# Performance work log

Measured on AMD Instinct MI355X. Metric: run time of the kernel, lower is better.

The kernel has to match this reference:

```python
import jax, jax.numpy as jnp
import numpy as np

R = 5            # num_relations
NEG_SLOPE = 0.2
N1 = 30000       # layer0 target count
N2 = 15000       # layer1 target count


def brgcn_conv(x_src, x_tgt, edge_index, edge_type, Wj, Wi, att_j, att_i,
               Wq, Wk, Wv, sw, sb, Wrel, heads, outc):
    """One BRGCNConv layer: per-relation GAT edge softmax + bilevel relation attention."""
    N = x_tgt.shape[0]
    hc = heads * outc
    hj = (x_src @ Wj).reshape(-1, heads, outc)   # [Ns,H,C]
    hi = (x_tgt @ Wi).reshape(-1, heads, outc)   # [N,H,C]
    src, tgt = edge_index[0], edge_index[1]
    xj = hj[src]                                  # [E,H,C]
    xi = hi[tgt]                                  # [E,H,C]
    # relation-specific attention logits per edge
    aj = jnp.sum(att_j[edge_type] * xj, axis=-1)  # [E,H]
    ai = jnp.sum(att_i[edge_type] * xi, axis=-1)  # [E,H]
    alpha = jax.nn.leaky_relu(aj + ai, NEG_SLOPE)
    # edge softmax grouped by (target node, relation) == per-relation propagate
    seg = tgt * R + edge_type                     # [E]
    nseg = N * R
    amax = jax.ops.segment_max(alpha, seg, num_segments=nseg)
    amax = jnp.where(jnp.isfinite(amax), amax, 0.0)
    ex = jnp.exp(alpha - amax[seg])
    den = jax.ops.segment_sum(ex, seg, num_segments=nseg)
    w = ex / jnp.maximum(den[seg], 1e-16)         # [E,H]
    msg = (w[:, :, None] * xj).reshape(-1, hc)    # [E,H*C]
    z = jax.ops.segment_sum(msg, seg, num_segments=nseg)
    z = z.reshape(N, R, hc).transpose(1, 0, 2)    # [R,N,H*C]; zero rows where no edges
    # per-relation Q/K/V
    q = jnp.einsum('rnd,rde->rne', z, Wq).reshape(R, N, heads, outc)
    k = jnp.einsum('rnd,rde->rne', z, Wk).reshape(R, N, heads, outc)
    v = jnp.einsum('rnd,rde->rne', z, Wv).reshape(R, N, heads, outc)
    # bilevel relation attention: psi[r,s,n,h] = <q_r, k_s>
    psi = jnp.einsum('rnhc,snhc->rsnh', q, k)
    mask = (psi == 0) & (jnp.sum(psi, axis=1, keepdims=True) != 0)
    prob = jax.nn.softmax(jnp.where(mask, -jnp.inf, psi), axis=1)
    delta = jnp.einsum('rsnh,snhc->rnhc', prob, v).reshape(R, N, hc)
    out = jnp.einsum('rnd,r->nd', delta, Wrel[:, 0])
    # single node type -> node_self[0] applied to every target node
    return out + x_tgt @ sw + sb


def setup_inputs() -> dict:
    key = jax.random.key(0)
    ks = jax.random.split(key, 32)
    H0, C0, H1, C1 = 4, 64, 1, 40
    IN, HC0 = 128, H0 * C0
    NG, N0 = 200000, 100000
    E0, E1 = 300000, 150000
    f = lambda k, s: jax.random.normal(k, s, dtype=jnp.float32) * 0.05
    return dict(
        n_id=jax.random.randint(ks[1], (N0,), 0, NG),
        local_node_idx=jax.random.randint(ks[2], (NG,), 0, NG),
        node_type=jnp.zeros((NG,), dtype=jnp.int32),
        edge_index0=jax.random.randint(ks[3], (2, E0), 0, N1),
        edge_type0=jax.random.randint(ks[4], (E0,), 0, R),
        edge_index1=jax.random.randint(ks[5], (2, E1), 0, N2),
        edge_type1=jax.random.randint(ks[6], (E1,), 0, R),
        emb=f(ks[0], (NG, IN)),
        Wj0=f(ks[7], (IN, HC0)), Wi0=f(ks[8], (IN, HC0)),
        att_j0=f(ks[9], (R, H0, C0)), att_i0=f(ks[10], (R, H0, C0)),
        Wq0=f(ks[11], (R, HC0, HC0)), Wk0=f(ks[12], (R, HC0, HC0)), Wv0=f(ks[13], (R, HC0, HC0)),
        sw0=f(ks[14], (IN, HC0)), sb0=f(ks[15], (HC0,)), Wrel0=f(ks[16], (R, 1)),
        Wj1=f(ks[17], (HC0, C1)), Wi1=f(ks[18], (HC0, C1)),
        att_j1=f(ks[19], (R, H1, C1)), att_i1=f(ks[20], (R, H1, C1)),
        Wq1=f(ks[21], (R, C1, C1)), Wk1=f(ks[22], (R, C1, C1)), Wv1=f(ks[23], (R, C1, C1)),
        sw1=f(ks[24], (HC0, C1)), sb1=f(ks[25], (C1,)), Wrel1=f(ks[26], (R, 1)),
    )


def reference(n_id, local_node_idx, node_type, edge_index0, edge_type0,
              edge_index1, edge_type1, emb,
              Wj0, Wi0, att_j0, att_i0, Wq0, Wk0, Wv0, sw0, sb0, Wrel0,
              Wj1, Wi1, att_j1, att_i1, Wq1, Wk1, Wv1, sw1, sb1, Wrel1):
    # group_input: single node type, all features from the embedding table
    x = emb[local_node_idx[n_id]]
    x1 = brgcn_conv(x, x[:N1], edge_index0, edge_type0, Wj0, Wi0, att_j0, att_i0,
                    Wq0, Wk0, Wv0, sw0, sb0, Wrel0, heads=4, outc=64)
    x1 = jax.nn.relu(x1)  # dropout p=0 in eval
    x2 = brgcn_conv(x1, x1[:N2], edge_index1, edge_type1, Wj1, Wi1, att_j1, att_i1,
                    Wq1, Wk1, Wv1, sw1, sb1, Wrel1, heads=1, outc=40)
    return jax.nn.log_softmax(x2, axis=-1)
```

## Files before the change

### kernel.cpp

```cpp
#include <hip/hip_runtime.h>
#include <hip/hip_bf16.h>

#define DI __device__ __forceinline__

DI float b2f(unsigned short u) {
    union { unsigned int i; float f; } x; x.i = ((unsigned int)u) << 16; return x.f;
}
DI unsigned short f2b(float f) {
    union { float f; unsigned int i; } x; x.f = f;
    unsigned int r = x.i + 0x7fff + ((x.i >> 16) & 1);
    return (unsigned short)(r >> 16);
}
DI float ldin(const void* p, long i, int f32) {
    return f32 ? ((const float*)p)[i] : b2f(((const unsigned short*)p)[i]);
}
DI void stval(float* p, float v) { *p = v; }
DI void stval(unsigned short* p, float v) { *p = f2b(v); }

static constexpr int N1 = 30000, N2 = 15000, R = 5;
static constexpr int IN = 128, HC0 = 256, C1 = 40;
static constexpr float NEGBIG = -1e30f;
static constexpr int LDK = 64;

typedef short bf16x8 __attribute__((ext_vector_type(8)));
typedef float f32x4 __attribute__((ext_vector_type(4)));

__global__ void detect_k(const void* emb, int* flag)
{
    int lane = threadIdx.x;
    int bad = 0;
    for (int j = 0; j < 4; ++j) {
        float f = b2f(((const unsigned short*)emb)[lane * 4 + j]);
        if (!(fabsf(f) < 1e8f)) bad = 1;
    }
    unsigned long long anybad = __ballot(bad != 0);
    if (lane == 0) *flag = (anybad != 0ull) ? 1 : 0;
}

struct PrepJobs {
    const void* src[12];
    unsigned short* dst[12];
    int K[12];
    int N[12];
    int per[12];
};
__global__ __launch_bounds__(256) void prep_all_k(
    PrepJobs J,
    const void* aj0, const void* ai0, const void* aj1, const void* ai1,
    unsigned short* A0j, unsigned short* A0i, unsigned short* A1j, unsigned short* A1i,
    int* __restrict__ cnt, int cntn,
    const int* __restrict__ dflag)
{
    const int f32 = *dflag;
    const int y = blockIdx.y;
    long t = (long)blockIdx.x * 256 + threadIdx.x;
    if (y < 12) {
        if (t >= J.per[y]) return;
        const int K = J.K[y], N = J.N[y];
        long kn = (long)K * N;
        long b = t / kn, rem = t % kn;
        long k = rem / N, n = rem % N;
        J.dst[y][(b * N + n) * K + k] = f2b(ldin(J.src[y], t, f32));
    } else {
        if (t < 20 * 256) {
            int j = (int)(t >> 8), k = (int)(t & 255);
            int h = j & 3, r = j >> 2;
            bool on = (k >> 6) == h;
            A0j[t] = f2b(on ? ldin(aj0, r * 256 + k, f32) : 0.f);
            A0i[t] = f2b(on ? ldin(ai0, r * 256 + k, f32) : 0.f);
        }
        if (t < 5 * 40) {
            A1j[t] = f2b(ldin(aj1, t, f32));
            A1i[t] = f2b(ldin(ai1, t, f32));
        }
        if (t < cntn) cnt[t] = 0;
    }
}

__global__ __launch_bounds__(256) void gather_k(
    const int* __restrict__ n_id, const int* __restrict__ lidx,
    const void* __restrict__ emb, unsigned short* __restrict__ x, int rows,
    const int* __restrict__ dflag)
{
    const int f32 = *dflag;
    long t = (long)blockIdx.x * 256 + threadIdx.x;
    long n = t >> 7, d = t & 127;
    if (n >= rows) return;
    long row = lidx[n_id[n]];
    x[n * IN + d] = f2b(ldin(emb, row * IN + d, f32));
}


DI void gload_lds16(const unsigned short* src, unsigned short* dst)
{
    __builtin_amdgcn_global_load_lds(
        (const __attribute__((address_space(1))) unsigned int*)src,
        (__attribute__((address_space(3))) unsigned int*)dst, 16, 0, 0);
}

DI void stage_fast(const unsigned short* __restrict__ G, int K,
                   unsigned short* S, int wave, int lane)
{
    const int p = lane >> 3;
    const int scol = ((lane & 7) ^ p) * 8;
#pragma unroll
    for (int t = 0; t < 4; ++t) {
        int row = t * 32 + wave * 8 + p;
        gload_lds16(G + (long)row * K + scol, S + (t * 32 + wave * 8) * LDK);
    }
}
DI void stage_fast8(const unsigned short* __restrict__ G, int K,
                    unsigned short* S, int wave, int lane)
{
    const int p = lane >> 3;
    const int scol = ((lane & 7) ^ p) * 8;
#pragma unroll
    for (int t = 0; t < 2; ++t) {
        int row = wave * 16 + t * 8 + p;
        gload_lds16(G + (long)row * K + scol, S + (wave * 16 + t * 8) * LDK);
    }
}
DI void stage_slow(const unsigned short* __restrict__ G, int rows, int K,
                   int r0, int k0, unsigned short* S, int tid)
{
    const int sr = tid >> 1, sq = (tid & 1) * 32;
    const int sx = sr & 7;
    unsigned short* drow = S + sr * LDK;
    const unsigned short* g = G + (long)(r0 + sr) * K + k0 + sq;
    const bool rowok = (r0 + sr) < rows;
    const int s0 = sq >> 3;
    if (rowok && (k0 + sq + 32) <= K) {
        const uint4* gv = (const uint4*)g;
        uint4 a = gv[0], b = gv[1], c = gv[2], d = gv[3];
        *(uint4*)(drow + (((s0 + 0) ^ sx) << 3)) = a;
        *(uint4*)(drow + (((s0 + 1) ^ sx) << 3)) = b;
        *(uint4*)(drow + (((s0 + 2) ^ sx) << 3)) = c;
        *(uint4*)(drow + (((s0 + 3) ^ sx) << 3)) = d;
    } else if (!rowok) {
        uint4 zz = {0u, 0u, 0u, 0u};
        *(uint4*)(drow + (((s0 + 0) ^ sx) << 3)) = zz;
        *(uint4*)(drow + (((s0 + 1) ^ sx) << 3)) = zz;
        *(uint4*)(drow + (((s0 + 2) ^ sx) << 3)) = zz;
        *(uint4*)(drow + (((s0 + 3) ^ sx) << 3)) = zz;
    } else {
#pragma unroll 8
        for (int j = 0; j < 32; ++j) {
            int col = sq + j;
            int k = k0 + col;
            int widx = (((col >> 3) ^ sx) << 3) | (col & 7);
            drow[widx] = (k < K) ? g[j] : (unsigned short)0;
        }
    }
}

template <int KK>
__global__ __launch_bounds__(512) void gemm_ares3_k(
    const unsigned short* __restrict__ Ab,
    const unsigned short* B0, const unsigned short* B1, const unsigned short* B2,
    unsigned short* C0, unsigned short* C1, unsigned short* C2,
    const void* bias0, const void* bias1, const void* bias2,
    const int* __restrict__ dflag,
    int M, long sA, long sB, long sC)
{
    __shared__ unsigned short As[128 * KK];
    __shared__ unsigned short Bs[2][128 * LDK];
    const int f32 = *dflag;
    const int tid = threadIdx.x;
    const int lane = tid & 63, wave = tid >> 6;
    const int b = blockIdx.z;
    const int n0 = blockIdx.x * 128, m0 = blockIdx.y * 128;
    const int wm = (wave & 1) * 64, wn = (wave >> 1) * 32;
    const int row16 = lane & 15, quad = lane >> 4;

    {
        const unsigned short* Gb = Ab + (long)b * sA + (long)m0 * KK;
        if (KK == 256) {
            const int lrow = lane >> 5, slin = lane & 31;
#pragma unroll
            for (int t = 0; t < 8; ++t) {
                int rbase = wave * 16 + t * 2;
                int row = rbase + lrow;
                gload_lds16(Gb + (long)row * 256 + ((slin ^ (row & 7)) << 3),
                            As + rbase * 256);
            }
        } else {
            const int lrow = lane >> 4, slin = lane & 15;
#pragma unroll
            for (int t = 0; t < 4; ++t) {
                int rbase = wave * 16 + t * 4;
                int row = rbase + lrow;
                gload_lds16(Gb + (long)row * 128 + ((slin ^ (row & 7)) << 3),
                            As + rbase * 128);
            }
        }
    }

    const unsigned short* Bbase[3] = {
        B0 + (long)b * sB + (long)n0 * KK,
        B1 + (long)b * sB + (long)n0 * KK,
        B2 + (long)b * sB + (long)n0 * KK };
    unsigned short* Cp[3] = { C0 + (long)b * sC, C1 + (long)b * sC, C2 + (long)b * sC };
    const void* biasp[3] = { bias0, bias1, bias2 };

    constexpr int NCH = KK / 64;
    constexpr int NQ = 3 * NCH;

    stage_fast8(Bbase[0], KK, Bs[0], wave, lane);
    asm volatile("s_waitcnt vmcnt(0)" ::: "memory");
    __builtin_amdgcn_s_barrier();
    asm volatile("" ::: "memory");

    int cur = 0;
    f32x4 acc[4][2];
#pragma unroll 1
    for (int q = 0; q < NQ; ++q) {
        const int sel = q / NCH, c = q % NCH;
        if (c == 0) {
#pragma unroll
            for (int i = 0; i < 4; ++i)
#pragma unroll
                for (int j = 0; j < 2; ++j) acc[i][j] = {0.f, 0.f, 0.f, 0.f};
        }
        if (q + 1 < NQ) {
            const int sel2 = (q + 1) / NCH, c2 = (q + 1) % NCH;
            stage_fast8(Bbase[sel2] + c2 * 64, KK, Bs[cur ^ 1], wave, lane);
            asm volatile("s_waitcnt vmcnt(2)" ::: "memory");
        } else {
            asm volatile("s_waitcnt vmcnt(0)" ::: "memory");
        }
        __builtin_amdgcn_s_barrier();
        asm volatile("" ::: "memory");
        const unsigned short* Bsc = Bs[cur];
#pragma unroll
        for (int ks = 0; ks < 64; ks += 32) {
            const int kk = c * 64 + ks;
            const int saw = ((((kk >> 3) + quad) ^ (row16 & 7)) << 3);
            const int sbw = ((((ks >> 3) + quad) ^ (row16 & 7)) << 3);
            bf16x8 af[4], bfr[2];
#pragma unroll
            for (int i = 0; i < 4; ++i)
                af[i] = *(const bf16x8*)(As + (wm + i * 16 + row16) * KK + saw);
#pragma unroll
            for (int j = 0; j < 2; ++j)
                bfr[j] = *(const bf16x8*)(Bsc + (wn + j * 16 + row16) * LDK + sbw);
#pragma unroll
            for (int i = 0; i < 4; ++i)
#pragma unroll
                for (int j = 0; j < 2; ++j)
                    acc[i][j] = __builtin_amdgcn_mfma_f32_16x16x32_bf16(
                        af[i], bfr[j], acc[i][j], 0, 0, 0);
        }
        asm volatile("" ::: "memory");
        __builtin_amdgcn_s_barrier();
        asm volatile("" ::: "memory");
        cur ^= 1;
        if (c == NCH - 1) {
            unsigned short* C = Cp[sel];
            const void* bias = biasp[sel];
#pragma unroll
            for (int i = 0; i < 4; ++i) {
#pragma unroll
                for (int reg = 0; reg < 4; ++reg) {
                    const int gr = m0 + wm + i * 16 + quad * 4 + reg;
                    if (gr >= M) continue;
#pragma unroll
                    for (int j = 0; j < 2; ++j) {
                        const int gc = n0 + wn + j * 16 + row16;
                        float v = acc[i][j][reg];
                        if (bias) v += ldin(bias, gc, f32);
                        C[(long)gr * 256 + gc] = f2b(v);
                    }
                }
            }
        }
    }
}

template <typename OT>
DI void gemm_mfma_body(
    const unsigned short* __restrict__ A, const unsigned short* __restrict__ Bt,
    OT* __restrict__ C, const void* __restrict__ bias, int f32,
    int M, int N, int K, unsigned short* As, unsigned short* Bs)
{
    const int tid = threadIdx.x;
    const int m0 = blockIdx.y * 128, n0 = blockIdx.x * 128;
    const int lane = tid & 63, wave = tid >> 6;
    const int wm = (wave & 1) * 64, wn = (wave >> 1) * 64;
    const int row16 = lane & 15, quad = lane >> 4;
    const bool kfull = (K & 63) == 0;
    const bool fastA = kfull && (m0 + 128 <= M);
    const bool fastB = kfull && (n0 + 128 <= N);
    f32x4 acc[4][4];
#pragma unroll
    for (int i = 0; i < 4; ++i)
#pragma unroll
        for (int j = 0; j < 4; ++j) acc[i][j] = {0.f, 0.f, 0.f, 0.f};

    for (int k0 = 0; k0 < K; k0 += 64) {
        if (fastA) stage_fast(A + (long)m0 * K + k0, K, As, wave, lane);
        else       stage_slow(A, M, K, m0, k0, As, tid);
        if (fastB) stage_fast(Bt + (long)n0 * K + k0, K, Bs, wave, lane);
        else       stage_slow(Bt, N, K, n0, k0, Bs, tid);
        __syncthreads();
#pragma unroll
        for (int ks = 0; ks < 64; ks += 32) {
            const int sw = (((quad + (ks >> 3)) ^ (row16 & 7)) << 3);
            bf16x8 af[4], bfr[4];
#pragma unroll
            for (int i = 0; i < 4; ++i)
                af[i] = *(const bf16x8*)(As + (wm + i * 16 + row16) * LDK + sw);
#pragma unroll
            for (int j = 0; j < 4; ++j)
                bfr[j] = *(const bf16x8*)(Bs + (wn + j * 16 + row16) * LDK + sw);
#pragma unroll
            for (int i = 0; i < 4; ++i)
#pragma unroll
                for (int j = 0; j < 4; ++j)
                    acc[i][j] = __builtin_amdgcn_mfma_f32_16x16x32_bf16(
                        af[i], bfr[j], acc[i][j], 0, 0, 0);
        }
        __syncthreads();
    }
#pragma unroll
    for (int i = 0; i < 4; ++i) {
#pragma unroll
        for (int reg = 0; reg < 4; ++reg) {
            const int gr = m0 + wm + i * 16 + quad * 4 + reg;
            if (gr >= M) continue;
#pragma unroll
            for (int j = 0; j < 4; ++j) {
                const int gc = n0 + wn + j * 16 + row16;
                if (gc >= N) continue;
                float v = acc[i][j][reg];
                if (bias) v += ldin(bias, gc, f32);
                stval(&C[(long)gr * N + gc], v);
            }
        }
    }
}

template <typename OT>
__global__ __launch_bounds__(256) void gemm_mfma3_k(
    const unsigned short* A0, const unsigned short* A1, const unsigned short* A2,
    const unsigned short* Bt0, const unsigned short* Bt1, const unsigned short* Bt2,
    OT* C0, OT* C1, OT* C2,
    const void* bias0, const void* bias1, const void* bias2,
    const int* __restrict__ dflag,
    int M, int N, int K, long sA, long sB, long sC, int nbatch)
{
    __shared__ unsigned short As[128 * LDK];
    __shared__ unsigned short Bs[128 * LDK];
    const int f32 = *dflag;
    const int sel = blockIdx.z / nbatch, b = blockIdx.z % nbatch;
    const unsigned short* A  = (sel == 0 ? A0 : sel == 1 ? A1 : A2) + (long)b * sA;
    const unsigned short* Bt = (sel == 0 ? Bt0 : sel == 1 ? Bt1 : Bt2) + (long)b * sB;
    OT* C = (sel == 0 ? C0 : sel == 1 ? C1 : C2) + (long)b * sC;
    const void* bias = sel == 0 ? bias0 : sel == 1 ? bias1 : bias2;
    gemm_mfma_body<OT>(A, Bt, C, bias, f32, M, N, K, As, Bs);
}

__global__ __launch_bounds__(256) void hist_k(const int* __restrict__ ei, int E, int* __restrict__ cnt)
{
    int e = blockIdx.x * 256 + threadIdx.x;
    if (e < E) atomicAdd(&cnt[ei[E + e]], 1);
}
__global__ __launch_bounds__(256) void scan1_k(
    const int* __restrict__ cnt, int* __restrict__ off, int* __restrict__ bsum, int n)
{
    __shared__ int buf[256];
    int i = blockIdx.x * 256 + threadIdx.x;
    int v = (i < n) ? cnt[i] : 0;
    buf[threadIdx.x] = v;
    __syncthreads();
#pragma unroll
    for (int s = 1; s < 256; s <<= 1) {
        int t = (threadIdx.x >= s) ? buf[threadIdx.x - s] : 0;
        __syncthreads();
        buf[threadIdx.x] += t;
        __syncthreads();
    }
    if (i < n) off[i] = buf[threadIdx.x] - v;
    if (threadIdx.x == 255) bsum[blockIdx.x] = buf[255];
}
__global__ void scan2_k(int* __restrict__ bsum, int nb, int* __restrict__ total_dst)
{
    __shared__ int buf[256];
    int v = (threadIdx.x < nb) ? bsum[threadIdx.x] : 0;
    buf[threadIdx.x] = v;
    __syncthreads();
#pragma unroll
    for (int s = 1; s < 256; s <<= 1) {
        int t = (threadIdx.x >= s) ? buf[threadIdx.x - s] : 0;
        __syncthreads();
        buf[threadIdx.x] += t;
        __syncthreads();
    }
    if (threadIdx.x < nb) bsum[threadIdx.x] = buf[threadIdx.x] - v;
    if (threadIdx.x == 255) *total_dst = buf[255];
}
__global__ __launch_bounds__(256) void scan3_k(
    int* __restrict__ off, int* __restrict__ cursor, const int* __restrict__ bsum,
    int* __restrict__ cnt, int n)
{
    int i = blockIdx.x * 256 + threadIdx.x;
    if (i < n) {
        int v = off[i] + bsum[blockIdx.x];
        off[i] = v;
        cursor[i] = v;
        cnt[i] = 0;
    }
}

__global__ __launch_bounds__(256) void scatter0_k(
    const int* __restrict__ ei, const int* __restrict__ et, int E,
    int* __restrict__ cursor,
    const float* __restrict__ ajn, const float* __restrict__ ain,
    int* __restrict__ src_s, int* __restrict__ rt_s, float* __restrict__ w4_s)
{
    int e = blockIdx.x * 256 + threadIdx.x;
    if (e >= E) return;
    int src = ei[e], tgt = ei[E + e], r = et[e];
    int p = atomicAdd(&cursor[tgt], 1);
    src_s[p] = src; rt_s[p] = r;
    float4 a = *(const float4*)(ajn + (long)src * 20 + r * 4);
    float4 b = *(const float4*)(ain + (long)tgt * 20 + r * 4);
    float4 w;
    float s0 = a.x + b.x, s1 = a.y + b.y, s2 = a.z + b.z, s3 = a.w + b.w;
    s0 = s0 > 0.f ? s0 : 0.2f * s0;  s1 = s1 > 0.f ? s1 : 0.2f * s1;
    s2 = s2 > 0.f ? s2 : 0.2f * s2;  s3 = s3 > 0.f ? s3 : 0.2f * s3;
    w.x = expf(fminf(s0, 60.f)); w.y = expf(fminf(s1, 60.f));
    w.z = expf(fminf(s2, 60.f)); w.w = expf(fminf(s3, 60.f));
    *(float4*)(w4_s + (long)p * 4) = w;
}
__global__ __launch_bounds__(256) void scatter1_k(
    const int* __restrict__ ei, const int* __restrict__ et, int E,
    int* __restrict__ cursor,
    const float* __restrict__ ajn, const float* __restrict__ ain,
    int* __restrict__ src_s, int* __restrict__ rt_s, float* __restrict__ w_s)
{
    int e = blockIdx.x * 256 + threadIdx.x;
    if (e >= E) return;
    int src = ei[e], tgt = ei[E + e], r = et[e];
    int p = atomicAdd(&cursor[tgt], 1);
    src_s[p] = src; rt_s[p] = r;
    float s = ajn[(long)src * 5 + r] + ain[(long)tgt * 5 + r];
    s = s > 0.f ? s : 0.2f * s;
    w_s[p] = expf(fminf(s, 60.f));
}

__global__ __launch_bounds__(256) void aggregate0_k(
    const int* __restrict__ src_s, const int* __restrict__ rt_s,
    const float* __restrict__ w4_s, const int* __restrict__ off,
    const unsigned short* __restrict__ hj,
    unsigned short* __restrict__ z, int Nn)
{
    int tgt = (int)((blockIdx.x * 256u + threadIdx.x) >> 6);
    int lane = threadIdx.x & 63;
    if (tgt >= Nn) return;
    int dd = lane * 4, h = lane >> 4;
    float acc[5][4] = {};
    float den[5] = {};
    int s = off[tgt], epd = off[tgt + 1];
    for (int i = s; i < epd; ++i) {
        int src = src_s[i];
        int r_e = rt_s[i];
        float wgt = w4_s[(long)i * 4 + h];
        ushort4 xj = *(const ushort4*)(hj + (long)src * 256 + dd);
        float x0 = b2f(xj.x), x1 = b2f(xj.y), x2 = b2f(xj.z), x3 = b2f(xj.w);
#pragma unroll
        for (int r = 0; r < 5; ++r) {
            float ws = (r == r_e) ? wgt : 0.f;
            den[r] += ws;
            acc[r][0] += ws * x0; acc[r][1] += ws * x1;
            acc[r][2] += ws * x2; acc[r][3] += ws * x3;
        }
    }
#pragma unroll
    for (int r = 0; r < 5; ++r) {
        float inv = 1.f / fmaxf(den[r], 1e-16f);
        ushort4 o;
        o.x = f2b(acc[r][0] * inv); o.y = f2b(acc[r][1] * inv);
        o.z = f2b(acc[r][2] * inv); o.w = f2b(acc[r][3] * inv);
        *(ushort4*)(z + ((long)r * Nn + tgt) * 256 + dd) = o;
    }
}

__global__ __launch_bounds__(256) void aggregate1_k(
    const int* __restrict__ src_s, const int* __restrict__ rt_s,
    const float* __restrict__ w_s, const int* __restrict__ off,
    const unsigned short* __restrict__ hj,
    unsigned short* __restrict__ z, int Nn)
{
    int tgt = (int)((blockIdx.x * 256u + threadIdx.x) >> 6);
    int lane = threadIdx.x & 63;
    if (tgt >= Nn) return;
    bool act = lane < 40;
    float acc[5] = {};
    float den[5] = {};
    int s = off[tgt], epd = off[tgt + 1];
    for (int i = s; i < epd; ++i) {
        int src = src_s[i];
        int r_e = rt_s[i];
        float wgt = w_s[i];
        float xj = act ? b2f(hj[(long)src * 40 + lane]) : 0.f;
#pragma unroll
        for (int r = 0; r < 5; ++r) {
            float ws = (r == r_e) ? wgt : 0.f;
            den[r] += ws;
            acc[r] += ws * xj;
        }
    }
    if (act) {
#pragma unroll
        for (int r = 0; r < 5; ++r) {
            float inv = 1.f / fmaxf(den[r], 1e-16f);
            z[((long)r * Nn + tgt) * 40 + lane] = f2b(acc[r] * inv);
        }
    }
}

__global__ __launch_bounds__(256) void fused_attn0_k(
    const unsigned short* __restrict__ qb, const unsigned short* __restrict__ kb,
    const unsigned short* __restrict__ vb, const void* __restrict__ wrel,
    unsigned short* __restrict__ x1, int n0, int nloc, int chq,
    const int* __restrict__ dflag)
{
    const int f32 = *dflag;
    int nl = (int)((blockIdx.x * 256u + threadIdx.x) >> 6);
    int lane = threadIdx.x & 63;
    if (nl >= nloc) return;
    int n = n0 + nl;
    int dd = lane * 4;
    float qf[5][4], kf[5][4];
#pragma unroll
    for (int r = 0; r < 5; ++r) {
        ushort4 qv = *(const ushort4*)(qb + ((long)r * chq + nl) * 256 + dd);
        ushort4 kv = *(const ushort4*)(kb + ((long)r * chq + nl) * 256 + dd);
        qf[r][0] = b2f(qv.x); qf[r][1] = b2f(qv.y); qf[r][2] = b2f(qv.z); qf[r][3] = b2f(qv.w);
        kf[r][0] = b2f(kv.x); kf[r][1] = b2f(kv.y); kf[r][2] = b2f(kv.z); kf[r][3] = b2f(kv.w);
    }
    float psi[5][5];
#pragma unroll
    for (int r = 0; r < 5; ++r)
#pragma unroll
        for (int s = 0; s < 5; ++s) {
            float p = qf[r][0] * kf[s][0] + qf[r][1] * kf[s][1] +
                      qf[r][2] * kf[s][2] + qf[r][3] * kf[s][3];
            p += __shfl_xor(p, 1, 64); p += __shfl_xor(p, 2, 64);
            p += __shfl_xor(p, 4, 64); p += __shfl_xor(p, 8, 64);
            psi[r][s] = p;
        }
    float pw[5] = {0.f, 0.f, 0.f, 0.f, 0.f};
#pragma unroll
    for (int r = 0; r < 5; ++r) {
        float rowsum = psi[r][0] + psi[r][1] + psi[r][2] + psi[r][3] + psi[r][4];
        float vals[5], m = NEGBIG;
#pragma unroll
        for (int s = 0; s < 5; ++s) {
            float v = (psi[r][s] == 0.f && rowsum != 0.f) ? NEGBIG : psi[r][s];
            vals[s] = v; m = fmaxf(m, v);
        }
        float es[5], sum = 0.f;
#pragma unroll
        for (int s = 0; s < 5; ++s) { es[s] = expf(vals[s] - m); sum += es[s]; }
        float wr = ldin(wrel, r, f32) / sum;
#pragma unroll
        for (int s = 0; s < 5; ++s) pw[s] += wr * es[s];
    }
    float acc[4] = {0.f, 0.f, 0.f, 0.f};
#pragma unroll
    for (int s = 0; s < 5; ++s) {
        ushort4 vv = *(const ushort4*)(vb + ((long)s * chq + nl) * 256 + dd);
        acc[0] += pw[s] * b2f(vv.x); acc[1] += pw[s] * b2f(vv.y);
        acc[2] += pw[s] * b2f(vv.z); acc[3] += pw[s] * b2f(vv.w);
    }
    ushort4* xp = (ushort4*)(x1 + (long)n * 256 + dd);
    ushort4 sv = *xp;
    sv.x = f2b(fmaxf(b2f(sv.x) + acc[0], 0.f));
    sv.y = f2b(fmaxf(b2f(sv.y) + acc[1], 0.f));
    sv.z = f2b(fmaxf(b2f(sv.z) + acc[2], 0.f));
    sv.w = f2b(fmaxf(b2f(sv.w) + acc[3], 0.f));
    *xp = sv;
}

__global__ __launch_bounds__(256) void fused_attn1_k(
    const unsigned short* __restrict__ qb, const unsigned short* __restrict__ kb,
    const unsigned short* __restrict__ vb, const void* __restrict__ wrel,
    const unsigned short* __restrict__ self1, void* __restrict__ out, int N,
    const int* __restrict__ dflag)
{
    const int f32 = *dflag;
    int n = (int)((blockIdx.x * 256u + threadIdx.x) >> 6);
    int lane = threadIdx.x & 63;
    if (n >= N) return;
    bool act = lane < 40;
    float qf[5], kf[5];
#pragma unroll
    for (int r = 0; r < 5; ++r) {
        long o = ((long)r * N + n) * 40 + lane;
        qf[r] = act ? b2f(qb[o]) : 0.f;
        kf[r] = act ? b2f(kb[o]) : 0.f;
    }
    float psi[5][5];
#pragma unroll
    for (int r = 0; r < 5; ++r)
#pragma unroll
        for (int s = 0; s < 5; ++s) {
            float p = qf[r] * kf[s];
            p += __shfl_xor(p, 1, 64);  p += __shfl_xor(p, 2, 64);
            p += __shfl_xor(p, 4, 64);  p += __shfl_xor(p, 8, 64);
            p += __shfl_xor(p, 16, 64); p += __shfl_xor(p, 32, 64);
            psi[r][s] = p;
        }
    float pw[5] = {0.f, 0.f, 0.f, 0.f, 0.f};
#pragma unroll
    for (int r = 0; r < 5; ++r) {
        float rowsum = psi[r][0] + psi[r][1] + psi[r][2] + psi[r][3] + psi[r][4];
        float vals[5], m = NEGBIG;
#pragma unroll
        for (int s = 0; s < 5; ++s) {
            float v = (psi[r][s] == 0.f && rowsum != 0.f) ? NEGBIG : psi[r][s];
            vals[s] = v; m = fmaxf(m, v);
        }
        float es[5], sum = 0.f;
#pragma unroll
        for (int s = 0; s < 5; ++s) { es[s] = expf(vals[s] - m); sum += es[s]; }
        float wr = ldin(wrel, r, f32) / sum;
#pragma unroll
        for (int s = 0; s < 5; ++s) pw[s] += wr * es[s];
    }
    float val = NEGBIG;
    if (act) {
        float acc = 0.f;
#pragma unroll
        for (int s = 0; s < 5; ++s) acc += pw[s] * b2f(vb[((long)s * N + n) * 40 + lane]);
        val = b2f(self1[(long)n * 40 + lane]) + acc;
    }
    float m = val;
#pragma unroll
    for (int msk = 1; msk < 64; msk <<= 1) m = fmaxf(m, __shfl_xor(m, msk, 64));
    float e = act ? expf(val - m) : 0.f;
#pragma unroll
    for (int msk = 1; msk < 64; msk <<= 1) e += __shfl_xor(e, msk, 64);
    if (act) {
        float r = val - m - logf(e);
        long oidx = (long)n * 40 + lane;
        if (f32) ((float*)out)[oidx] = r;
        else     ((unsigned short*)out)[oidx] = f2b(r);
    }
}

extern "C" void kernel_launch(void* const* d_in, const int* in_sizes, int n_in,
                              void* d_out, int out_size, void* d_ws, size_t ws_size,
                              hipStream_t stream)
{
    const int* n_id = (const int*)d_in[0];
    const int* lidx = (const int*)d_in[1];
    const int* ei0  = (const int*)d_in[3];
    const int* et0  = (const int*)d_in[4];
    const int* ei1  = (const int*)d_in[5];
    const int* et1  = (const int*)d_in[6];
    const void* emb = d_in[7];
    const void* Wj0 = d_in[8];  const void* Wi0 = d_in[9];
    const void* aj0 = d_in[10]; const void* ai0 = d_in[11];
    const void* Wq0 = d_in[12]; const void* Wk0 = d_in[13]; const void* Wv0 = d_in[14];
    const void* sw0 = d_in[15]; const void* sb0 = d_in[16]; const void* Wr0 = d_in[17];
    const void* Wj1 = d_in[18]; const void* Wi1 = d_in[19];
    const void* aj1 = d_in[20]; const void* ai1 = d_in[21];
    const void* Wq1 = d_in[22]; const void* Wk1 = d_in[23]; const void* Wv1 = d_in[24];
    const void* sw1 = d_in[25]; const void* sb1 = d_in[26]; const void* Wr1 = d_in[27];
    const int E0 = in_sizes[4], E1 = in_sizes[6];

    auto al = [](size_t b) { return (b + 255) & ~(size_t)255; };

    const size_t P_total =
        al((size_t)R * N1 * HC0 * 2) +
        al((size_t)N1 * HC0 * 2) +
        2 * al((size_t)N1 * 20 * 4) +
        3 * al((size_t)(N1 + 1) * 4) +
        al(256 * 4) +
        2 * al((size_t)E0 * 4) +
        al((size_t)E0 * 16) +
        3 * al((size_t)HC0 * IN * 2) +
        3 * al((size_t)R * HC0 * HC0 * 2) +
        3 * al((size_t)C1 * HC0 * 2) +
        3 * al((size_t)R * C1 * C1 * 2) +
        2 * al(20 * 256 * 2) + 2 * al(5 * 40 * 2) +
        al(256);

    int CH = 15000;
    {
        size_t need = 3 * al((size_t)R * CH * HC0 * 2) + P_total + (16u << 20);
        if (need > ws_size) CH = 7500;
    }
    const size_t QB = al((size_t)R * CH * HC0 * 2);

    char* w = (char*)d_ws;
    unsigned short* qc = (unsigned short*)(w);
    unsigned short* kc = (unsigned short*)(w + QB);
    unsigned short* vc = (unsigned short*)(w + 2 * QB);
    unsigned short* x30k = (unsigned short*)(w);
    unsigned short* hj0  = (unsigned short*)(w + al((size_t)N1 * IN * 2));
    unsigned short* hi0  = (unsigned short*)((char*)hj0 + al((size_t)N1 * HC0 * 2));
    size_t o1 = 0;
    auto take1 = [&](size_t b) { char* p = w + o1; o1 += (b + 255) & ~(size_t)255; return p; };
    unsigned short* hj1   = (unsigned short*)take1((size_t)N2 * C1 * 2);
    unsigned short* hi1   = (unsigned short*)take1((size_t)N2 * C1 * 2);
    unsigned short* self1 = (unsigned short*)take1((size_t)N2 * C1 * 2);
    float* ajn1 = (float*)take1((size_t)N2 * R * 4);
    float* ain1 = (float*)take1((size_t)N2 * R * 4);
    unsigned short* z1  = (unsigned short*)take1((size_t)R * N2 * C1 * 2);
    unsigned short* q1b = (unsigned short*)take1((size_t)R * N2 * C1 * 2);
    unsigned short* k1b = (unsigned short*)take1((size_t)R * N2 * C1 * 2);
    unsigned short* v1b = (unsigned short*)take1((size_t)R * N2 * C1 * 2);
    size_t o = 3 * QB;
    auto take = [&](size_t b) { char* p = w + o; o += (b + 255) & ~(size_t)255; return p; };
    unsigned short* z0 = (unsigned short*)take((size_t)R * N1 * HC0 * 2);
    unsigned short* x1 = (unsigned short*)take((size_t)N1 * HC0 * 2);
    float* ajn0 = (float*)take((size_t)N1 * 20 * 4);
    float* ain0 = (float*)take((size_t)N1 * 20 * 4);
    int* cnt    = (int*)take((size_t)(N1 + 1) * 4);
    int* off    = (int*)take((size_t)(N1 + 1) * 4);
    int* cursor = (int*)take((size_t)(N1 + 1) * 4);
    int* bsum   = (int*)take(256 * 4);
    int* src_s  = (int*)take((size_t)E0 * 4);
    int* rt_s   = (int*)take((size_t)E0 * 4);
    float* w4_s = (float*)take((size_t)E0 * 16);
    unsigned short* wjt0 = (unsigned short*)take((size_t)HC0 * IN * 2);
    unsigned short* wit0 = (unsigned short*)take((size_t)HC0 * IN * 2);
    unsigned short* swt0 = (unsigned short*)take((size_t)HC0 * IN * 2);
    unsigned short* wqt0 = (unsigned short*)take((size_t)R * HC0 * HC0 * 2);
    unsigned short* wkt0 = (unsigned short*)take((size_t)R * HC0 * HC0 * 2);
    unsigned short* wvt0 = (unsigned short*)take((size_t)R * HC0 * HC0 * 2);
    unsigned short* wjt1 = (unsigned short*)take((size_t)C1 * HC0 * 2);
    unsigned short* wit1 = (unsigned short*)take((size_t)C1 * HC0 * 2);
    unsigned short* swt1 = (unsigned short*)take((size_t)C1 * HC0 * 2);
    unsigned short* wqt1 = (unsigned short*)take((size_t)R * C1 * C1 * 2);
    unsigned short* wkt1 = (unsigned short*)take((size_t)R * C1 * C1 * 2);
    unsigned short* wvt1 = (unsigned short*)take((size_t)R * C1 * C1 * 2);
    unsigned short* atA0j = (unsigned short*)take(20 * 256 * 2);
    unsigned short* atA0i = (unsigned short*)take(20 * 256 * 2);
    unsigned short* atA1j = (unsigned short*)take(5 * 40 * 2);
    unsigned short* atA1i = (unsigned short*)take(5 * 40 * 2);
    int* dflag = (int*)take(256);

    detect_k<<<1, 64, 0, stream>>>(emb, dflag);

    {
        PrepJobs J;
        const void* srcs[12] = {Wj0, Wi0, sw0, Wq0, Wk0, Wv0, Wj1, Wi1, sw1, Wq1, Wk1, Wv1};
        unsigned short* dsts[12] = {wjt0, wit0, swt0, wqt0, wkt0, wvt0,
                                    wjt1, wit1, swt1, wqt1, wkt1, wvt1};
        int Ks[12] = {IN, IN, IN, HC0, HC0, HC0, HC0, HC0, HC0, C1, C1, C1};
        int Ns[12] = {HC0, HC0, HC0, HC0, HC0, HC0, C1, C1, C1, C1, C1, C1};
        int pers[12] = {IN * HC0, IN * HC0, IN * HC0,
                        R * HC0 * HC0, R * HC0 * HC0, R * HC0 * HC0,
                        HC0 * C1, HC0 * C1, HC0 * C1,
                        R * C1 * C1, R * C1 * C1, R * C1 * C1};
        for (int i = 0; i < 12; ++i) {
            J.src[i] = srcs[i]; J.dst[i] = dsts[i];
            J.K[i] = Ks[i]; J.N[i] = Ns[i]; J.per[i] = pers[i];
        }
        int xb = (R * HC0 * HC0 + 255) / 256;
        prep_all_k<<<dim3((unsigned)xb, 13), 256, 0, stream>>>(
            J, aj0, ai0, aj1, ai1, atA0j, atA0i, atA1j, atA1i, cnt, N1 + 1, dflag);
    }

    gather_k<<<(int)(((long)N1 * IN + 255) / 256), 256, 0, stream>>>(n_id, lidx, emb, x30k, N1, dflag);
    gemm_ares3_k<128><<<dim3(2, (N1 + 127) / 128, 1), 512, 0, stream>>>(
        x30k, wjt0, wit0, swt0, hj0, hi0, x1, nullptr, nullptr, sb0,
        dflag, N1, 0, 0, 0);
    gemm_mfma3_k<float><<<dim3(1, (N1 + 127) / 128, 2), 256, 0, stream>>>(
        hj0, hi0, hi0, atA0j, atA0i, atA0i, ajn0, ain0, ain0, nullptr, nullptr, nullptr,
        dflag, N1, 20, HC0, 0, 0, 0, 1);

    hist_k<<<(E0 + 255) / 256, 256, 0, stream>>>(ei0, E0, cnt);
    {
        int nb = (N1 + 255) / 256;
        scan1_k<<<nb, 256, 0, stream>>>(cnt, off, bsum, N1);
        scan2_k<<<1, 256, 0, stream>>>(bsum, nb, off + N1);
        scan3_k<<<nb, 256, 0, stream>>>(off, cursor, bsum, cnt, N1);
    }
    scatter0_k<<<(E0 + 255) / 256, 256, 0, stream>>>(ei0, et0, E0, cursor, ajn0, ain0, src_s, rt_s, w4_s);
    aggregate0_k<<<(N1 + 3) / 4, 256, 0, stream>>>(src_s, rt_s, w4_s, off, hj0, z0, N1);

    {
        const int nch = N1 / CH;
        for (int c = 0; c < nch; ++c) {
            const unsigned short* zc = z0 + (long)c * CH * HC0;
            gemm_ares3_k<256><<<dim3(2, (CH + 127) / 128, R), 512, 0, stream>>>(
                zc, wqt0, wkt0, wvt0, qc, kc, vc, nullptr, nullptr, nullptr,
                dflag, CH, (long)N1 * HC0, (long)HC0 * HC0, (long)CH * HC0);
            fused_attn0_k<<<(CH + 3) / 4, 256, 0, stream>>>(qc, kc, vc, Wr0, x1, c * CH, CH, CH, dflag);
        }
    }

    gemm_mfma3_k<unsigned short><<<dim3(1, (N2 + 127) / 128, 3), 256, 0, stream>>>(
        x1, x1, x1, wjt1, wit1, swt1, hj1, hi1, self1, nullptr, nullptr, sb1,
        dflag, N2, C1, HC0, 0, 0, 0, 1);
    gemm_mfma3_k<float><<<dim3(1, (N2 + 127) / 128, 2), 256, 0, stream>>>(
        hj1, hi1, hi1, atA1j, atA1i, atA1i, ajn1, ain1, ain1, nullptr, nullptr, nullptr,
        dflag, N2, 5, C1, 0, 0, 0, 1);

    hist_k<<<(E1 + 255) / 256, 256, 0, stream>>>(ei1, E1, cnt);
    {
        int nb = (N2 + 255) / 256;
        scan1_k<<<nb, 256, 0, stream>>>(cnt, off, bsum, N2);
        scan2_k<<<1, 256, 0, stream>>>(bsum, nb, off + N2);
        scan3_k<<<nb, 256, 0, stream>>>(off, cursor, bsum, cnt, N2);
    }
    scatter1_k<<<(E1 + 255) / 256, 256, 0, stream>>>(ei1, et1, E1, cursor, ajn1, ain1, src_s, rt_s, w4_s);
    aggregate1_k<<<(N2 + 3) / 4, 256, 0, stream>>>(src_s, rt_s, w4_s, off, hj1, z1, N2);

    {
        long sA = (long)N2 * C1, sB = (long)C1 * C1, sC = (long)N2 * C1;
        gemm_mfma3_k<unsigned short><<<dim3(1, (N2 + 127) / 128, 3 * R), 256, 0, stream>>>(
            z1, z1, z1, wqt1, wkt1, wvt1, q1b, k1b, v1b, nullptr, nullptr, nullptr,
            dflag, N2, C1, C1, sA, sB, sC, R);
    }
    fused_attn1_k<<<(N2 + 3) / 4, 256, 0, stream>>>(q1b, k1b, v1b, Wr1, self1, d_out, N2, dflag);
}
```

Baseline: 673.5 us.

## Replace double-buffered B staging with single-buffer syncthreads loop in 3-output GEMM

Rewrites the A-resident triple-output GEMM so B tiles are staged into one LDS buffer per 64-wide K chunk, with __syncthreads around each compute step. The old flattened software pipeline prefetched the next chunk while computing the current one. The new version halves B shared memory, which may raise occupancy or simplify scheduling, but global loads no longer overlap with MFMA work.

```diff
diff --git a/kernel.cpp b/kernel.cpp
--- a/kernel.cpp
+++ b/kernel.cpp
@@ -154,7 +154,7 @@
 }
 
 template <int KK>
-__global__ __launch_bounds__(512) void gemm_ares3_k(
+__global__ __launch_bounds__(512) void gemm_ares4_k(
     const unsigned short* __restrict__ Ab,
     const unsigned short* B0, const unsigned short* B1, const unsigned short* B2,
     unsigned short* C0, unsigned short* C1, unsigned short* C2,
@@ -163,7 +163,7 @@
     int M, long sA, long sB, long sC)
 {
     __shared__ unsigned short As[128 * KK];
-    __shared__ unsigned short Bs[2][128 * LDK];
+    __shared__ unsigned short Bs[128 * LDK];
     const int f32 = *dflag;
     const int tid = threadIdx.x;
     const int lane = tid & 63, wave = tid >> 6;
@@ -195,81 +195,54 @@
         }
     }
 
-    const unsigned short* Bbase[3] = {
-        B0 + (long)b * sB + (long)n0 * KK,
-        B1 + (long)b * sB + (long)n0 * KK,
-        B2 + (long)b * sB + (long)n0 * KK };
-    unsigned short* Cp[3] = { C0 + (long)b * sC, C1 + (long)b * sC, C2 + (long)b * sC };
-    const void* biasp[3] = { bias0, bias1, bias2 };
-
-    constexpr int NCH = KK / 64;
-    constexpr int NQ = 3 * NCH;
-
-    stage_fast8(Bbase[0], KK, Bs[0], wave, lane);
-    asm volatile("s_waitcnt vmcnt(0)" ::: "memory");
-    __builtin_amdgcn_s_barrier();
-    asm volatile("" ::: "memory");
-
-    int cur = 0;
-    f32x4 acc[4][2];
 #pragma unroll 1
-    for (int q = 0; q < NQ; ++q) {
-        const int sel = q / NCH, c = q % NCH;
-        if (c == 0) {
-#pragma unroll
-            for (int i = 0; i < 4; ++i)
-#pragma unroll
-                for (int j = 0; j < 2; ++j) acc[i][j] = {0.f, 0.f, 0.f, 0.f};
-        }
-        if (q + 1 < NQ) {
-            const int sel2 = (q + 1) / NCH, c2 = (q + 1) % NCH;
-            stage_fast8(Bbase[sel2] + c2 * 64, KK, Bs[cur ^ 1], wave, lane);
-            asm volatile("s_waitcnt vmcnt(2)" ::: "memory");
-        } else {
-            asm volatile("s_waitcnt vmcnt(0)" ::: "memory");
-        }
-        __builtin_amdgcn_s_barrier();
-        asm volatile("" ::: "memory");
-        const unsigned short* Bsc = Bs[cur];
-#pragma unroll
-        for (int ks = 0; ks < 64; ks += 32) {
-            const int kk = c * 64 + ks;
-            const int saw = ((((kk >> 3) + quad) ^ (row16 & 7)) << 3);
-            const int sbw = ((((ks >> 3) + quad) ^ (row16 & 7)) << 3);
-            bf16x8 af[4], bfr[2];
-#pragma unroll
-            for (int i = 0; i < 4; ++i)
-                af[i] = *(const bf16x8*)(As + (wm + i * 16 + row16) * KK + saw);
-#pragma unroll
-            for (int j = 0; j < 2; ++j)
-                bfr[j] = *(const bf16x8*)(Bsc + (wn + j * 16 + row16) * LDK + sbw);
-#pragma unroll
-            for (int i = 0; i < 4; ++i)
+    for (int sel = 0; sel < 3; ++sel) {
+        const unsigned short* Bt = (sel == 0 ? B0 : sel == 1 ? B1 : B2)
+                                   + (long)b * sB + (long)n0 * KK;
+        unsigned short* C = (sel == 0 ? C0 : sel == 1 ? C1 : C2) + (long)b * sC;
+        const void* bias = sel == 0 ? bias0 : sel == 1 ? bias1 : bias2;
+        f32x4 acc[4][2];
+#pragma unroll
+        for (int i = 0; i < 4; ++i)
+#pragma unroll
+            for (int j = 0; j < 2; ++j) acc[i][j] = {0.f, 0.f, 0.f, 0.f};
+
+        for (int k0 = 0; k0 < KK; k0 += 64) {
+            stage_fast8(Bt + k0, KK, Bs, wave, lane);
+            __syncthreads();
+#pragma unroll
+            for (int ks = 0; ks < 64; ks += 32) {
+                const int kk = k0 + ks;
+                const int saw = ((((kk >> 3) + quad) ^ (row16 & 7)) << 3);
+                const int sbw = ((((ks >> 3) + quad) ^ (row16 & 7)) << 3);
+                bf16x8 af[4], bfr[2];
+#pragma unroll
+                for (int i = 0; i < 4; ++i)
+                    af[i] = *(const bf16x8*)(As + (wm + i * 16 + row16) * KK + saw);
 #pragma unroll
                 for (int j = 0; j < 2; ++j)
-                    acc[i][j] = __builtin_amdgcn_mfma_f32_16x16x32_bf16(
-                        af[i], bfr[j], acc[i][j], 0, 0, 0);
-        }
-        asm volatile("" ::: "memory");
-        __builtin_amdgcn_s_barrier();
-        asm volatile("" ::: "memory");
-        cur ^= 1;
-        if (c == NCH - 1) {
-            unsigned short* C = Cp[sel];
-            const void* bias = biasp[sel];
-#pragma unroll
-            for (int i = 0; i < 4; ++i) {
-#pragma unroll
-                for (int reg = 0; reg < 4; ++reg) {
-                    const int gr = m0 + wm + i * 16 + quad * 4 + reg;
-                    if (gr >= M) continue;
-#pragma unroll
-                    for (int j = 0; j < 2; ++j) {
-                        const int gc = n0 + wn + j * 16 + row16;
-                        float v = acc[i][j][reg];
-                        if (bias) v += ldin(bias, gc, f32);
-                        C[(long)gr * 256 + gc] = f2b(v);
-                    }
+                    bfr[j] = *(const bf16x8*)(Bs + (wn + j * 16 + row16) * LDK + sbw);
+#pragma unroll
+                for (int i = 0; i < 4; ++i)
+#pragma unroll
+                    for (int j = 0; j < 2; ++j)
+                        acc[i][j] = __builtin_amdgcn_mfma_f32_16x16x32_bf16(
+                            af[i], bfr[j], acc[i][j], 0, 0, 0);
+            }
+            __syncthreads();
+        }
+#pragma unroll
+        for (int i = 0; i < 4; ++i) {
+#pragma unroll
+            for (int reg = 0; reg < 4; ++reg) {
+                const int gr = m0 + wm + i * 16 + quad * 4 + reg;
+                if (gr >= M) continue;
+#pragma unroll
+                for (int j = 0; j < 2; ++j) {
+                    const int gc = n0 + wn + j * 16 + row16;
+                    float v = acc[i][j][reg];
+                    if (bias) v += ldin(bias, gc, f32);
+                    C[(long)gr * 256 + gc] = f2b(v);
                 }
             }
         }
@@ -767,7 +740,7 @@
     }
 
     gather_k<<<(int)(((long)N1 * IN + 255) / 256), 256, 0, stream>>>(n_id, lidx, emb, x30k, N1, dflag);
-    gemm_ares3_k<128><<<dim3(2, (N1 + 127) / 128, 1), 512, 0, stream>>>(
+    gemm_ares4_k<128><<<dim3(2, (N1 + 127) / 128, 1), 512, 0, stream>>>(
         x30k, wjt0, wit0, swt0, hj0, hi0, x1, nullptr, nullptr, sb0,
         dflag, N1, 0, 0, 0);
     gemm_mfma3_k<float><<<dim3(1, (N1 + 127) / 128, 2), 256, 0, stream>>>(
@@ -788,7 +761,7 @@
         const int nch = N1 / CH;
         for (int c = 0; c < nch; ++c) {
             const unsigned short* zc = z0 + (long)c * CH * HC0;
-            gemm_ares3_k<256><<<dim3(2, (CH + 127) / 128, R), 512, 0, stream>>>(
+            gemm_ares4_k<256><<<dim3(2, (CH + 127) / 128, R), 512, 0, stream>>>(
                 zc, wqt0, wkt0, wvt0, qc, kc, vc, nullptr, nullptr, nullptr,
                 dflag, CH, (long)N1 * HC0, (long)HC0 * HC0, (long)CH * HC0);
             fused_attn0_k<<<(CH + 3) / 4, 256, 0, stream>>>(qc, kc, vc, Wr0, x1, c * CH, CH, CH, dflag);
```

New measurement: 617.9 us. 8.2% less time.
